# Kernel tuning notes

Measured on AMD Instinct MI355X. Metric: run time of the kernel, lower is better.

## Reference

```python
import jax, jax.numpy as jnp
import numpy as np

B, S, HID = 4, 1024, 4096
NH, NKV, HD = 32, 8, 128
FF = 11008
EPS = 1e-6
THETA = 10000.0


def rms_norm(x, w, eps=EPS):
    v = jnp.mean(jnp.square(x), axis=-1, keepdims=True)
    return x * jax.lax.rsqrt(v + eps) * w


def rotate_half(x):
    x1, x2 = jnp.split(x, 2, axis=-1)
    return jnp.concatenate([-x2, x1], axis=-1)


def rope_cos_sin(position_ids, head_dim=HD, theta=THETA):
    inv_freq = 1.0 / (theta ** (jnp.arange(0, head_dim, 2, dtype=jnp.float32) / head_dim))
    freqs = position_ids.astype(jnp.float32)[..., None] * inv_freq  # [B,S,HD/2]
    emb = jnp.concatenate([freqs, freqs], axis=-1)  # [B,S,HD]
    return jnp.cos(emb)[:, None, :, :], jnp.sin(emb)[:, None, :, :]  # [B,1,S,HD]


def setup_inputs() -> dict:
    key = jax.random.key(0)
    ks = jax.random.split(key, 9)
    sc = 0.02
    pos = jnp.tile(jnp.arange(S, dtype=jnp.int64 if jax.config.jax_enable_x64 else jnp.int32)[None, :], (B, 1))
    causal = jnp.tril(jnp.ones((S, S), dtype=bool))
    mask = jnp.where(causal, 0.0, -1e9).astype(jnp.float32)[None, None]  # [1,1,S,S]
    return {
        "hidden_states": jax.random.normal(ks[0], (B * S, HID), jnp.float32),
        "position_ids": pos,
        "attn_mask": mask,
        "Wq": jax.random.normal(ks[1], (HID, NH * HD), jnp.float32) * sc,
        "Wk": jax.random.normal(ks[2], (HID, NKV * HD), jnp.float32) * sc,
        "Wv": jax.random.normal(ks[3], (HID, NKV * HD), jnp.float32) * sc,
        "Wo": jax.random.normal(ks[4], (NH * HD, HID), jnp.float32) * sc,
        "ln1_w": jnp.ones((HID,), jnp.float32),
        "ln2_w": jnp.ones((HID,), jnp.float32),
        "w_gate": jax.random.normal(ks[5], (HID, FF), jnp.float32) * sc,
        "w_up": jax.random.normal(ks[6], (HID, FF), jnp.float32) * sc,
        "w_down": jax.random.normal(ks[7], (FF, HID), jnp.float32) * sc,
    }


def reference(hidden_states, position_ids, attn_mask, Wq, Wk, Wv, Wo, ln1_w, ln2_w, w_gate, w_up, w_down):
    residual = hidden_states
    h = rms_norm(hidden_states, ln1_w)

    # QKV projections on flat tokens, then reshape per train partition
    q = (h @ Wq).reshape(B, S, NH, HD).transpose(0, 2, 1, 3)     # [B,NH,S,HD]
    k = (h @ Wk).reshape(B, S, NKV, HD).transpose(0, 2, 1, 3)    # [B,NKV,S,HD]
    v = (h @ Wv).reshape(B, S, NKV, HD).transpose(0, 2, 1, 3)

    cos, sin = rope_cos_sin(position_ids)
    q = q * cos + rotate_half(q) * sin
    k = k * cos + rotate_half(k) * sin

    n_rep = NH // NKV
    k = jnp.repeat(k, n_rep, axis=1)  # [B,NH,S,HD]
    v = jnp.repeat(v, n_rep, axis=1)

    scores = jnp.einsum('bhqd,bhkd->bhqk', q, k) / np.sqrt(HD)
    scores = scores + attn_mask
    # softmax in fp32 as in the source
    probs = jax.nn.softmax(scores.astype(jnp.float32), axis=-1).astype(q.dtype)
    attn = jnp.einsum('bhqk,bhkd->bhqd', probs, v)               # [B,NH,S,HD]
    attn = attn.transpose(0, 2, 1, 3).reshape(B * S, NH * HD)
    h = attn @ Wo

    h = residual + h
    residual = h
    h2 = rms_norm(h, ln2_w)
    mlp = (jax.nn.silu(h2 @ w_gate) * (h2 @ w_up)) @ w_down
    return residual + mlp
```

## Files before the change

kernel.cpp:

```cpp
#include <hip/hip_runtime.h>

#define DEVINL __device__ __forceinline__

typedef unsigned short u16;
typedef __attribute__((ext_vector_type(8))) short bf16x8;
typedef __attribute__((ext_vector_type(4))) float f32x4;
typedef __attribute__((ext_vector_type(4))) unsigned short u16x4;


DEVINL float bf2f(u16 u) { union { unsigned i; float f; } x; x.i = ((unsigned)u) << 16; return x.f; }
DEVINL u16 f2bf(float f) {
  union { float f; unsigned i; } x; x.f = f;
  unsigned r = x.i + 0x7fffu + ((x.i >> 16) & 1u);
  return (u16)(r >> 16);
}

DEVINL void async16(u16* lds, const u16* g) {
  __builtin_amdgcn_global_load_lds((const __attribute__((address_space(1))) unsigned*)g,
                                   (__attribute__((address_space(3))) unsigned*)lds, 16, 0, 0);
}

struct CJob { const float* in; u16* out; int K, N, ntiles; };

DEVINL void conv_one(const float* __restrict__ in, u16* __restrict__ out,
                     int K, int N, int tile, int t, float (*tl)[65]) {
  int tn = N >> 6;
  int kt = tile / tn;
  int k0 = kt << 6, n0 = (tile - kt*tn) << 6;
  int r = t >> 4, c4 = (t & 15) << 2;
  #pragma unroll
  for (int it = 0; it < 4; it++) {
    int row = r + it*16;
    f32x4 v = *(const f32x4*)(in + (size_t)(k0 + row)*N + n0 + c4);
    tl[row][c4+0] = v[0]; tl[row][c4+1] = v[1];
    tl[row][c4+2] = v[2]; tl[row][c4+3] = v[3];
  }
  __syncthreads();
  #pragma unroll
  for (int it = 0; it < 4; it++) {
    int nrow = r + it*16;
    u16x4 ov;
    #pragma unroll
    for (int e = 0; e < 4; e++) ov[e] = f2bf(tl[c4+e][nrow]);
    *(u16x4*)(out + (size_t)(n0 + nrow)*K + k0 + c4) = ov;
  }
  __syncthreads();
}

__global__ __launch_bounds__(256) void conv3(CJob j0, CJob j1, CJob j2) {
  __shared__ float tl[64][65];
  int ntot = j0.ntiles + j1.ntiles + j2.ntiles;
  for (int g = blockIdx.x; g < ntot; g += gridDim.x) {
    const float* in; u16* out; int K, N, tile;
    if (g < j0.ntiles)                 { in = j0.in; out = j0.out; K = j0.K; N = j0.N; tile = g; }
    else if (g < j0.ntiles + j1.ntiles){ in = j1.in; out = j1.out; K = j1.K; N = j1.N; tile = g - j0.ntiles; }
    else                               { in = j2.in; out = j2.out; K = j2.K; N = j2.N; tile = g - j0.ntiles - j1.ntiles; }
    conv_one(in, out, K, N, tile, threadIdx.x, tl);
  }
}

__global__ __launch_bounds__(256) void conv_t(const float* __restrict__ in,
                                              u16* __restrict__ out, int K, int N) {
  __shared__ float tl[64][65];
  int tile = blockIdx.y * gridDim.x + blockIdx.x;
  conv_one(in, out, K, N, tile, threadIdx.x, tl);
}

__global__ __launch_bounds__(256) void rmsnorm_kernel(const float* __restrict__ x,
                                                      const float* __restrict__ w,
                                                      u16* __restrict__ out) {
  int row = blockIdx.x, t = threadIdx.x;
  const float* xr = x + (size_t)row * 4096;
  f32x4 v[4];
  float ss = 0.f;
  #pragma unroll
  for (int i = 0; i < 4; i++) {
    v[i] = *(const f32x4*)(xr + (t + 256*i)*4);
    ss += v[i][0]*v[i][0] + v[i][1]*v[i][1] + v[i][2]*v[i][2] + v[i][3]*v[i][3];
  }
  #pragma unroll
  for (int d = 1; d < 64; d <<= 1) ss += __shfl_xor(ss, d, 64);
  __shared__ float ps[4];
  if ((t & 63) == 0) ps[t >> 6] = ss;
  __syncthreads();
  float scale = rsqrtf((ps[0]+ps[1]+ps[2]+ps[3]) * (1.f/4096.f) + 1e-6f);
  #pragma unroll
  for (int i = 0; i < 4; i++) {
    f32x4 wv = *(const f32x4*)(w + (t + 256*i)*4);
    u16x4 o;
    #pragma unroll
    for (int e = 0; e < 4; e++) o[e] = f2bf(v[i][e] * scale * wv[e]);
    *(u16x4*)(out + (size_t)row*4096 + (t + 256*i)*4) = o;
  }
}

__global__ __launch_bounds__(256) void rope_kernel(u16* __restrict__ q, u16* __restrict__ k, int kstr) {
  int tok = blockIdx.x;
  int s = tok & 1023;
  __shared__ float cs[64], sn[64];
  int t = threadIdx.x;
  if (t < 64) {
    float inv = __expf(-(float)t * 0.14391156934f);
    float ang = (float)s * inv;
    cs[t] = cosf(ang); sn[t] = sinf(ang);
  }
  __syncthreads();
  const float qscale = 0.08838834764831845f;
  size_t qbase = (size_t)tok * 4096;
  #pragma unroll
  for (int it = 0; it < 8; it++) {
    int item = t + it*256; int h = item >> 6, j = item & 63;
    size_t i0 = qbase + h*128 + j;
    float x1 = bf2f(q[i0]), x2 = bf2f(q[i0+64]);
    float c = cs[j], si = sn[j];
    q[i0]    = f2bf((x1*c - x2*si) * qscale);
    q[i0+64] = f2bf((x2*c + x1*si) * qscale);
  }
  size_t kbase = (size_t)tok * kstr;
  #pragma unroll
  for (int it = 0; it < 2; it++) {
    int item = t + it*256; int h = item >> 6, j = item & 63;
    size_t i0 = kbase + h*128 + j;
    float x1 = bf2f(k[i0]), x2 = bf2f(k[i0+64]);
    float c = cs[j], si = sn[j];
    k[i0]    = f2bf(x1*c - x2*si);
    k[i0+64] = f2bf(x2*c + x1*si);
  }
}

__global__ __launch_bounds__(256) void vtrans(const u16* __restrict__ v, u16* __restrict__ vt, int vstr) {
  __shared__ u16 tile[32][33];
  int bh = blockIdx.z; int b = bh >> 3, kvh = bh & 7;
  int d0 = blockIdx.x << 5, s0 = blockIdx.y << 5;
  int tx = threadIdx.x, ty = threadIdx.y;
  for (int r = ty; r < 32; r += 8)
    tile[r][tx] = v[(size_t)(b*1024 + s0 + r)*vstr + kvh*128 + d0 + tx];
  __syncthreads();
  for (int r = ty; r < 32; r += 8)
    vt[(size_t)((b*8 + kvh)*128 + d0 + r)*1024 + s0 + tx] = tile[tx][r];
}

template<int EPI>
__global__ __launch_bounds__(256, 2) void gemm_bt(
    const u16* __restrict__ A, const u16* __restrict__ Bt,
    void* __restrict__ Cv, const float* __restrict__ resid,
    const u16* __restrict__ gate, int M, int N, int K) {
  __shared__ u16 As[128*64];
  __shared__ u16 Bs[128*64];
  int nwg = gridDim.x;
  int bid = (int)blockIdx.x;
  int cpx = nwg >> 3;
  int swz = (bid & 7) * cpx + (bid >> 3);
  int mt = M >> 7;
  int m0 = (swz % mt) << 7;
  int n0 = (swz / mt) << 7;
  int tid = threadIdx.x;
  int lane = tid & 63, wave = tid >> 6;
  int wm = wave >> 1, wn = wave & 1;

  f32x4 acc[4][4];
  f32x4 zero = {0.f, 0.f, 0.f, 0.f};
  #pragma unroll
  for (int i = 0; i < 4; i++)
    #pragma unroll
    for (int j = 0; j < 4; j++) acc[i][j] = zero;

  int arow[4], acolb[4];
  #pragma unroll
  for (int i = 0; i < 4; i++) {
    int c = i*256 + tid;
    arow[i]  = c >> 3;
    acolb[i] = ((c & 7) * 16) ^ ((arow[i] & 7) << 4);
  }

  int nsteps = K >> 6;
  for (int t = 0; t < nsteps; t++) {
    int k0 = t << 6;
    #pragma unroll
    for (int i = 0; i < 4; i++) {
      async16(As + i*2048 + wave*512, A  + (size_t)(m0 + arow[i])*K + k0 + (acolb[i] >> 1));
      async16(Bs + i*2048 + wave*512, Bt + (size_t)(n0 + arow[i])*K + k0 + (acolb[i] >> 1));
    }
    __syncthreads();
    #pragma unroll
    for (int ks = 0; ks < 2; ks++) {
      bf16x8 af[4], bfr[4];
      int c2 = (ks*32 + (lane >> 4)*8) * 2;
      #pragma unroll
      for (int mf = 0; mf < 4; mf++) {
        int r = wm*64 + mf*16 + (lane & 15);
        af[mf] = *(const bf16x8*)(As + r*64 + ((c2 ^ ((r & 7) << 4)) >> 1));
      }
      #pragma unroll
      for (int nf = 0; nf < 4; nf++) {
        int r = wn*64 + nf*16 + (lane & 15);
        bfr[nf] = *(const bf16x8*)(Bs + r*64 + ((c2 ^ ((r & 7) << 4)) >> 1));
      }
      #pragma unroll
      for (int mf = 0; mf < 4; mf++)
        #pragma unroll
        for (int nf = 0; nf < 4; nf++)
          acc[mf][nf] = __builtin_amdgcn_mfma_f32_16x16x32_bf16(af[mf], bfr[nf], acc[mf][nf], 0, 0, 0);
    }
    __syncthreads();
  }

  #pragma unroll
  for (int mf = 0; mf < 4; mf++)
    #pragma unroll
    for (int nf = 0; nf < 4; nf++)
      #pragma unroll
      for (int j = 0; j < 4; j++) {
        int rr = m0 + wm*64 + mf*16 + (lane >> 4)*4 + j;
        int cc = n0 + wn*64 + nf*16 + (lane & 15);
        size_t idx = (size_t)rr * N + cc;
        float v = acc[mf][nf][j];
        if constexpr (EPI == 0) {
          ((u16*)Cv)[idx] = f2bf(v);
        } else if constexpr (EPI == 1) {
          ((float*)Cv)[idx] = v + resid[idx];
        } else {
          float g = bf2f(gate[idx]);
          float sg = g / (1.f + __expf(-g));
          ((u16*)Cv)[idx] = f2bf(sg * v);
        }
      }
}

#define SB0() __builtin_amdgcn_sched_barrier(0)
#define BAR() __builtin_amdgcn_s_barrier()
#define LGKM(n) do { SB0(); asm volatile("s_waitcnt lgkmcnt(" #n ")" ::: "memory"); SB0(); } while (0)
#define VMC(n)  do { SB0(); asm volatile("s_waitcnt vmcnt(" #n ")"  ::: "memory"); SB0(); } while (0)
#define MFMAQ(qm, qn, AF, BQ) do { \
  __builtin_amdgcn_s_setprio(1); \
  _Pragma("unroll") for (int mf_ = 0; mf_ < 4; mf_++) \
  _Pragma("unroll") for (int nf_ = 0; nf_ < 2; nf_++) \
  _Pragma("unroll") for (int ks_ = 0; ks_ < 2; ks_++) \
    acc[(qm)*4+mf_][(qn)*2+nf_] = __builtin_amdgcn_mfma_f32_16x16x32_bf16( \
        AF[mf_][ks_], BQ[nf_][ks_], acc[(qm)*4+mf_][(qn)*2+nf_], 0, 0, 0); \
  __builtin_amdgcn_s_setprio(0); } while (0)

template<int KC, int EPI>
__global__ __launch_bounds__(512, 2) void gemm256(
    const u16* __restrict__ A, const u16* __restrict__ Bt,
    void* __restrict__ Cv, const float* __restrict__ resid,
    const u16* __restrict__ gate, int M, int N, int G,
    const float* __restrict__ cvin, u16* __restrict__ cvout, int cvK, int cvN, int cvTiles) {
  extern __shared__ u16 lds[];
  int bid = (int)blockIdx.x;
  int tid = threadIdx.x;

  if (bid >= G) {
    int cb = bid - G, CB = (int)gridDim.x - G;
    int h = tid >> 8, t = tid & 255;
    float (*tl)[65] = (float(*)[65])((char*)lds + h*16896);
    int pairs = cvTiles >> 1;
    for (int p = cb; p < pairs; p += CB)
      conv_one(cvin, cvout, cvK, cvN, 2*p + h, t, tl);
    return;
  }

  int cpx = G >> 3;
  int swz = (bid & 7) * cpx + (bid >> 3);
  int mt = M >> 8;
  int m0 = (swz % mt) << 8;
  int n0 = (swz / mt) << 8;
  int lane = tid & 63, wave = tid >> 6;
  int wm = wave >> 2, wn = wave & 3;

  f32x4 acc[8][4];
  f32x4 zero = {0.f, 0.f, 0.f, 0.f};
  #pragma unroll
  for (int i = 0; i < 8; i++)
    #pragma unroll
    for (int j = 0; j < 4; j++) acc[i][j] = zero;

  int sCol = ((lane & 7) ^ (lane >> 3)) << 3;
  int aRow = (wave >> 2)*128 + (wave & 3)*16 + (lane >> 3);
  int bRow = (wave >> 1)*64  + (wave & 1)*16 + (lane >> 3);
  const u16* gA = A  + (size_t)(m0 + aRow) * KC + sCol;
  const u16* gB = Bt + (size_t)(n0 + bRow) * KC + sCol;
  constexpr size_t K8 = (size_t)8 * KC, K32 = (size_t)32 * KC, K64 = (size_t)64 * KC;

  int rA = lane & 15;
  int acol0 = (((lane >> 4)    ) ^ (rA & 7)) << 3;
  int acol1 = (((lane >> 4) + 4) ^ (rA & 7)) << 3;

  bf16x8 afA[4][2], afB[4][2], b0[2][2], b1[2][2];

  auto stageAq = [&](int buf, int qm, int k0) {
    u16* d = lds + buf*32768 + qm*8192 + wave*1024;
    const u16* s = gA + (size_t)qm*K64 + k0;
    async16(d, s); async16(d + 512, s + K8);
  };
  auto stageBq = [&](int buf, int qn, int k0) {
    u16* d = lds + buf*32768 + 16384 + qn*8192 + wave*1024;
    const u16* s = gB + (size_t)qn*K32 + k0;
    async16(d, s); async16(d + 512, s + K8);
  };
  auto loadAq = [&](int buf, int qm, bf16x8 (&af)[4][2]) {
    const u16* base = lds + buf*32768 + qm*8192 + wm*4096 + rA*64;
    #pragma unroll
    for (int mf = 0; mf < 4; mf++) {
      af[mf][0] = *(const bf16x8*)(base + mf*1024 + acol0);
      af[mf][1] = *(const bf16x8*)(base + mf*1024 + acol1);
    }
  };
  auto loadBq = [&](int buf, int qn, bf16x8 (&bq)[2][2]) {
    const u16* base = lds + buf*32768 + 16384 + qn*8192 + wn*2048 + rA*64;
    #pragma unroll
    for (int nf = 0; nf < 2; nf++) {
      bq[nf][0] = *(const bf16x8*)(base + nf*1024 + acol0);
      bq[nf][1] = *(const bf16x8*)(base + nf*1024 + acol1);
    }
  };

  constexpr int nt = KC >> 6;
  constexpr int IT = nt/2 - 1;

  stageAq(0, 0, 0); stageBq(0, 0, 0); stageBq(0, 1, 0); stageAq(0, 1, 0);
  VMC(4);
  stageAq(1, 0, 64); stageBq(1, 0, 64); stageBq(1, 1, 64);
  VMC(6);
  BAR();

  #pragma unroll 1
  for (int it = 0; it < IT; it++) {
    int kc = it*128;
    loadAq(0, 0, afA); loadBq(0, 0, b0); stageAq(1, 1, kc + 64);
    LGKM(8); BAR(); LGKM(0);
    MFMAQ(0, 0, afA, b0);
    SB0(); BAR();
    loadBq(0, 1, b1); stageAq(0, 0, kc + 128);
    BAR(); LGKM(0);
    MFMAQ(0, 1, afA, b1);
    SB0(); BAR();
    loadAq(0, 1, afB); stageBq(0, 0, kc + 128);
    BAR(); LGKM(0);
    MFMAQ(1, 0, afB, b0);
    SB0(); BAR();
    stageBq(0, 1, kc + 128);
    BAR();
    MFMAQ(1, 1, afB, b1);
    VMC(6); BAR();
    loadAq(1, 0, afA); loadBq(1, 0, b0); stageAq(0, 1, kc + 128);
    LGKM(8); BAR(); LGKM(0);
    MFMAQ(0, 0, afA, b0);
    SB0(); BAR();
    loadBq(1, 1, b1); stageAq(1, 0, kc + 192);
    BAR(); LGKM(0);
    MFMAQ(0, 1, afA, b1);
    SB0(); BAR();
    loadAq(1, 1, afB); stageBq(1, 0, kc + 192);
    BAR(); LGKM(0);
    MFMAQ(1, 0, afB, b0);
    SB0(); BAR();
    stageBq(1, 1, kc + 192);
    BAR();
    MFMAQ(1, 1, afB, b1);
    VMC(6); BAR();
  }

  {
    int kc = IT*128;
    loadAq(0, 0, afA); loadBq(0, 0, b0); stageAq(1, 1, kc + 64);
    LGKM(8); BAR(); LGKM(0);
    MFMAQ(0, 0, afA, b0);
    SB0(); BAR();
    loadBq(0, 1, b1);
    BAR(); LGKM(0);
    MFMAQ(0, 1, afA, b1);
    SB0(); BAR();
    loadAq(0, 1, afB);
    BAR(); LGKM(0);
    MFMAQ(1, 0, afB, b0);
    SB0(); BAR();
    MFMAQ(1, 1, afB, b1);
    VMC(0); BAR();
    loadAq(1, 0, afA); loadBq(1, 0, b0); SB0();
    loadBq(1, 1, b1); SB0();
    loadAq(1, 1, afB); SB0();
    LGKM(12); MFMAQ(0, 0, afA, b0);
    LGKM(8);  MFMAQ(0, 1, afA, b1);
    LGKM(0);  MFMAQ(1, 0, afB, b0);
    MFMAQ(1, 1, afB, b1);
  }

  #pragma unroll
  for (int mf = 0; mf < 8; mf++)
    #pragma unroll
    for (int nf = 0; nf < 4; nf++)
      #pragma unroll
      for (int j = 0; j < 4; j++) {
        int rr = m0 + wm*128 + mf*16 + (lane >> 4)*4 + j;
        int cc = n0 + wn*64 + nf*16 + (lane & 15);
        size_t idx = (size_t)rr * N + cc;
        float v = acc[mf][nf][j];
        if constexpr (EPI == 0) {
          ((u16*)Cv)[idx] = f2bf(v);
        } else if constexpr (EPI == 1) {
          ((float*)Cv)[idx] = v + resid[idx];
        } else {
          float g = bf2f(gate[idx]);
          float sg = g / (1.f + __expf(-g));
          ((u16*)Cv)[idx] = f2bf(sg * v);
        }
      }
}

__global__ __launch_bounds__(256, 4) void attn_kernel(
    const u16* __restrict__ q, const u16* __restrict__ k,
    const u16* __restrict__ vt, u16* __restrict__ out,
    CJob j0, CJob j1, CJob j2, int kstr) {
  __shared__ __align__(16) u16 shm[20480];
  u16* Ks = shm;
  u16* Vs = shm + 8192;
  u16* Ps = shm + 16384;
  int bid = blockIdx.x;

  if (bid >= 2048) {
    int cb = bid - 2048, CB = (int)gridDim.x - 2048;
    float (*tl)[65] = (float(*)[65])shm;
    int ntot = j0.ntiles + j1.ntiles + j2.ntiles;
    for (int g = cb; g < ntot; g += CB) {
      const float* in; u16* outp; int K, N, tile;
      if (g < j0.ntiles)                  { in = j0.in; outp = j0.out; K = j0.K; N = j0.N; tile = g; }
      else if (g < j0.ntiles + j1.ntiles) { in = j1.in; outp = j1.out; K = j1.K; N = j1.N; tile = g - j0.ntiles; }
      else                                { in = j2.in; outp = j2.out; K = j2.K; N = j2.N; tile = g - j0.ntiles - j1.ntiles; }
      conv_one(in, outp, K, N, tile, threadIdx.x, tl);
    }
    return;
  }

  int qt = bid & 15;
  int h  = (bid >> 4) & 31;
  int b  = bid >> 9;
  int kvh = h >> 2;
  int tid = threadIdx.x, lane = tid & 63, wave = tid >> 6;
  int q0 = qt << 6;

  bf16x8 qf[4];
  {
    const u16* qb_ = q + (size_t)(b*1024 + q0 + wave*16 + (lane & 15))*4096 + h*128 + (lane >> 4)*8;
    #pragma unroll
    for (int ks = 0; ks < 4; ks++) qf[ks] = *(const bf16x8*)(qb_ + ks*32);
  }
  f32x4 o[8];
  f32x4 zero = {0.f,0.f,0.f,0.f};
  #pragma unroll
  for (int i = 0; i < 8; i++) o[i] = zero;
  float m[4] = {-1e30f,-1e30f,-1e30f,-1e30f};
  float l[4] = {0.f,0.f,0.f,0.f};

  int kr[4], kc[4], vr[4], vc[4];
  #pragma unroll
  for (int i = 0; i < 4; i++) {
    int c = i*256 + tid;
    kr[i] = c >> 4; kc[i] = ((c & 15)*16) ^ ((kr[i] & 7) << 4);
    vr[i] = c >> 3; vc[i] = ((c & 7)*16)  ^ ((vr[i] & 7) << 4);
  }

  for (int t = 0; t <= qt; t++) {
    int kv0 = t << 6;
    #pragma unroll
    for (int i = 0; i < 4; i++) {
      async16(Ks + i*2048 + wave*512, k  + (size_t)(b*1024 + kv0 + kr[i])*kstr + kvh*128 + (kc[i] >> 1));
      async16(Vs + i*2048 + wave*512, vt + (size_t)((b*8 + kvh)*128 + vr[i])*1024 + kv0 + (vc[i] >> 1));
    }
    __syncthreads();

    f32x4 s[4];
    #pragma unroll
    for (int nf = 0; nf < 4; nf++) {
      s[nf] = zero;
      #pragma unroll
      for (int ks = 0; ks < 4; ks++) {
        int r = nf*16 + (lane & 15);
        int c2 = (ks*32 + (lane >> 4)*8)*2;
        bf16x8 kf = *(const bf16x8*)(Ks + r*128 + ((c2 ^ ((r & 7) << 4)) >> 1));
        s[nf] = __builtin_amdgcn_mfma_f32_16x16x32_bf16(qf[ks], kf, s[nf], 0, 0, 0);
      }
    }
    if (t == qt) {
      #pragma unroll
      for (int nf = 0; nf < 4; nf++)
        #pragma unroll
        for (int j = 0; j < 4; j++) {
          int cc = nf*16 + (lane & 15);
          int rr = wave*16 + (lane >> 4)*4 + j;
          if (cc > rr) s[nf][j] = -1e30f;
        }
    }
    #pragma unroll
    for (int j = 0; j < 4; j++) {
      float mx = fmaxf(fmaxf(s[0][j], s[1][j]), fmaxf(s[2][j], s[3][j]));
      #pragma unroll
      for (int d = 1; d < 16; d <<= 1) mx = fmaxf(mx, __shfl_xor(mx, d, 64));
      float mn = fmaxf(m[j], mx);
      float f = __expf(m[j] - mn);
      m[j] = mn;
      float ssum = 0.f;
      #pragma unroll
      for (int nf = 0; nf < 4; nf++) {
        float p = __expf(s[nf][j] - mn);
        s[nf][j] = p; ssum += p;
      }
      #pragma unroll
      for (int d = 1; d < 16; d <<= 1) ssum += __shfl_xor(ssum, d, 64);
      l[j] = l[j]*f + ssum;
      #pragma unroll
      for (int nf = 0; nf < 8; nf++) o[nf][j] *= f;
    }
    #pragma unroll
    for (int nf = 0; nf < 4; nf++)
      #pragma unroll
      for (int j = 0; j < 4; j++) {
        int rr = (lane >> 4)*4 + j;
        int cb2 = ((nf*16 + (lane & 15))*2) ^ ((rr & 7) << 4);
        Ps[wave*1024 + rr*64 + (cb2 >> 1)] = f2bf(s[nf][j]);
      }
    #pragma unroll
    for (int ks2 = 0; ks2 < 2; ks2++) {
      int mr = lane & 15;
      int c2 = (ks2*32 + (lane >> 4)*8)*2;
      bf16x8 pa = *(const bf16x8*)(Ps + wave*1024 + mr*64 + ((c2 ^ ((mr & 7) << 4)) >> 1));
      #pragma unroll
      for (int nf = 0; nf < 8; nf++) {
        int d = nf*16 + (lane & 15);
        bf16x8 vf = *(const bf16x8*)(Vs + d*64 + ((c2 ^ ((d & 7) << 4)) >> 1));
        o[nf] = __builtin_amdgcn_mfma_f32_16x16x32_bf16(pa, vf, o[nf], 0, 0, 0);
      }
    }
    __syncthreads();
  }

  float inv[4];
  #pragma unroll
  for (int j = 0; j < 4; j++) inv[j] = 1.f / l[j];
  u16* ob = out + (size_t)(b*1024 + q0 + wave*16)*4096 + h*128;
  #pragma unroll
  for (int nf = 0; nf < 8; nf++)
    #pragma unroll
    for (int j = 0; j < 4; j++) {
      int rr = (lane >> 4)*4 + j;
      int cc = nf*16 + (lane & 15);
      ob[(size_t)rr*4096 + cc] = f2bf(o[nf][j] * inv[j]);
    }
}

extern "C" void kernel_launch(void* const* d_in, const int* in_sizes, int n_in,
                              void* d_out, int out_size, void* d_ws, size_t ws_size,
                              hipStream_t stream) {
  (void)in_sizes; (void)n_in; (void)out_size;
  const float* hidden = (const float*)d_in[0];
  const float* Wq  = (const float*)d_in[3];
  const float* Wk  = (const float*)d_in[4];
  const float* Wv  = (const float*)d_in[5];
  const float* Wo  = (const float*)d_in[6];
  const float* ln1 = (const float*)d_in[7];
  const float* ln2 = (const float*)d_in[8];
  const float* Wg  = (const float*)d_in[9];
  const float* Wu  = (const float*)d_in[10];
  const float* Wd  = (const float*)d_in[11];
  float* out = (float*)d_out;

  hipFuncSetAttribute((const void*)gemm256<4096,0>,  hipFuncAttributeMaxDynamicSharedMemorySize, 131072);
  hipFuncSetAttribute((const void*)gemm256<4096,1>,  hipFuncAttributeMaxDynamicSharedMemorySize, 131072);
  hipFuncSetAttribute((const void*)gemm256<4096,2>,  hipFuncAttributeMaxDynamicSharedMemorySize, 131072);
  hipFuncSetAttribute((const void*)gemm256<11008,1>, hipFuncAttributeMaxDynamicSharedMemorySize, 131072);

  char* ws = (char*)d_ws;
  size_t off = 0;
  auto alloc = [&](size_t b) { char* p = ws + off; off += (b + 4095) & ~(size_t)4095; return p; };

  u16*  wqkvT = (u16*)alloc(50331648);
  u16*  woT   = (u16*)alloc(33554432);
  u16*  wgT   = (u16*)alloc(90177536);
  u16*  wuT   = (u16*)alloc(90177536);
  u16*  h1    = (u16*)alloc(33554432);
  u16*  qb    = (u16*)alloc(33554432);
  u16*  kvb   = (u16*)alloc(16777216);
  u16*  vtb   = (u16*)alloc(8388608);
  float* hmid = (float*)alloc(67108864);
  u16*  gb    = (u16*)alloc(90177536);
  bool fused = off <= ws_size;

  dim3 blk(256);
  if (fused) {
    u16* wqT  = wqkvT;
    u16* wkvT = wqkvT + 16777216;
    u16* wkT  = wkvT;
    u16* wvT  = wkvT + 4194304;
    u16* wdT  = wgT;
    CJob Jq{Wq, wqT, 4096, 4096, 4096}, Jk{Wk, wkT, 4096, 1024, 1024}, Jv{Wv, wvT, 4096, 1024, 1024};
    CJob Jo{Wo, woT, 4096, 4096, 4096}, Jg{Wg, wgT, 4096, 11008, 11008}, Ju{Wu, wuT, 4096, 11008, 11008};

    conv3<<<2048, blk, 0, stream>>>(Jq, Jk, Jv);
    rmsnorm_kernel<<<4096, blk, 0, stream>>>(hidden, ln1, h1);
    gemm256<4096,0><<<256, 512, 131072, stream>>>(h1, wqT, qb, nullptr, nullptr, 4096, 4096, 256,
                                                  nullptr, nullptr, 0, 0, 0);
    gemm_bt<0><<<512, blk, 0, stream>>>(h1, wkvT, kvb, nullptr, nullptr, 4096, 2048, 4096);
    rope_kernel<<<4096, blk, 0, stream>>>(qb, kvb, 2048);
    vtrans<<<dim3(4, 32, 32), dim3(32, 8), 0, stream>>>(kvb + 1024, vtb, 2048);
    attn_kernel<<<2048 + 1024, blk, 0, stream>>>(qb, kvb, vtb, h1, Jo, Jg, Ju, 2048);
    gemm256<4096,1><<<256, 512, 131072, stream>>>(h1, woT, hmid, hidden, nullptr, 4096, 4096, 256,
                                                  nullptr, nullptr, 0, 0, 0);
    rmsnorm_kernel<<<4096, blk, 0, stream>>>(hmid, ln2, qb);
    gemm256<4096,0><<<688, 512, 131072, stream>>>(qb, wgT, gb, nullptr, nullptr, 4096, 11008, 688,
                                                  nullptr, nullptr, 0, 0, 0);
    gemm256<4096,2><<<688 + 344, 512, 131072, stream>>>(qb, wuT, gb, nullptr, gb, 4096, 11008, 688,
                                                        Wd, wdT, 11008, 4096, 11008);
    gemm256<11008,1><<<256, 512, 131072, stream>>>(gb, wdT, out, hmid, nullptr, 4096, 4096, 256,
                                                   nullptr, nullptr, 0, 0, 0);
  } else {
    off = 0;
    u16*  W1   = (u16*)alloc(90177536);
    u16*  h1s  = (u16*)alloc(33554432);
    u16*  qbs  = (u16*)alloc(33554432);
    u16*  kvbs = (u16*)alloc(16777216);
    u16*  vtbs = (u16*)alloc(8388608);
    float* hmids = (float*)alloc(67108864);
    u16*  gbs  = (u16*)alloc(90177536);
    if (off > ws_size) return;
    u16* wqT  = W1;
    u16* wkvT = W1 + 16777216;
    conv_t<<<dim3(64, 64),  blk, 0, stream>>>(Wq, wqT, 4096, 4096);
    conv_t<<<dim3(16, 64),  blk, 0, stream>>>(Wk, wkvT, 4096, 1024);
    conv_t<<<dim3(16, 64),  blk, 0, stream>>>(Wv, wkvT + 4194304, 4096, 1024);
    rmsnorm_kernel<<<4096, blk, 0, stream>>>(hidden, ln1, h1s);
    gemm256<4096,0><<<256, 512, 131072, stream>>>(h1s, wqT, qbs, nullptr, nullptr, 4096, 4096, 256,
                                                  nullptr, nullptr, 0, 0, 0);
    gemm_bt<0><<<512, blk, 0, stream>>>(h1s, wkvT, kvbs, nullptr, nullptr, 4096, 2048, 4096);
    rope_kernel<<<4096, blk, 0, stream>>>(qbs, kvbs, 2048);
    vtrans<<<dim3(4, 32, 32), dim3(32, 8), 0, stream>>>(kvbs + 1024, vtbs, 2048);
    CJob J0{nullptr, nullptr, 0, 64, 0};
    attn_kernel<<<2048, blk, 0, stream>>>(qbs, kvbs, vtbs, h1s, J0, J0, J0, 2048);
    conv_t<<<dim3(64, 64), blk, 0, stream>>>(Wo, W1, 4096, 4096);
    gemm256<4096,1><<<256, 512, 131072, stream>>>(h1s, W1, hmids, hidden, nullptr, 4096, 4096, 256,
                                                  nullptr, nullptr, 0, 0, 0);
    rmsnorm_kernel<<<4096, blk, 0, stream>>>(hmids, ln2, qbs);
    conv_t<<<dim3(172, 64), blk, 0, stream>>>(Wg, W1, 4096, 11008);
    gemm256<4096,0><<<688, 512, 131072, stream>>>(qbs, W1, gbs, nullptr, nullptr, 4096, 11008, 688,
                                                  nullptr, nullptr, 0, 0, 0);
    conv_t<<<dim3(172, 64), blk, 0, stream>>>(Wu, W1, 4096, 11008);
    gemm256<4096,2><<<688, 512, 131072, stream>>>(qbs, W1, gbs, nullptr, gbs, 4096, 11008, 688,
                                                  nullptr, nullptr, 0, 0, 0);
    conv_t<<<dim3(64, 172), blk, 0, stream>>>(Wd, W1, 11008, 4096);
    gemm256<11008,1><<<256, 512, 131072, stream>>>(gbs, W1, out, hmids, nullptr, 4096, 4096, 256,
                                                   nullptr, nullptr, 0, 0, 0);
  }
}
```

Before: 1.665 ms.

## Fuse gate and up projections into one GEMM with interleaved weights

Gate and up weights are converted into a single interleaved buffer, alternating 32-row blocks, so that one GEMM of width 22016 produces both projections in the same tile. A new epilogue applies SiLU(gate)*up directly from registers. This removes the separate gate GEMM, its bf16 write of the gate result and the later read-back. The cost is a larger combined weight buffer and a reshuffled workspace layout, with the down-weight conversion now placed in the QKV buffer region.

```diff
diff --git a/kernel.cpp b/kernel.cpp
--- a/kernel.cpp
+++ b/kernel.cpp
@@ -20,10 +20,10 @@
                                    (__attribute__((address_space(3))) unsigned*)lds, 16, 0, 0);
 }
 
-struct CJob { const float* in; u16* out; int K, N, ntiles; };
+struct CJob { const float* in; u16* out; int K, N, ntiles; int mode; };
 
 DEVINL void conv_one(const float* __restrict__ in, u16* __restrict__ out,
-                     int K, int N, int tile, int t, float (*tl)[65]) {
+                     int K, int N, int tile, int t, float (*tl)[65], int mode) {
   int tn = N >> 6;
   int kt = tile / tn;
   int k0 = kt << 6, n0 = (tile - kt*tn) << 6;
@@ -42,7 +42,10 @@
     u16x4 ov;
     #pragma unroll
     for (int e = 0; e < 4; e++) ov[e] = f2bf(tl[c4+e][nrow]);
-    *(u16x4*)(out + (size_t)(n0 + nrow)*K + k0 + c4) = ov;
+    int orow = n0 + nrow;
+    if (mode == 1)      orow = ((orow >> 5) << 6) + (orow & 31);
+    else if (mode == 2) orow = ((orow >> 5) << 6) + 32 + (orow & 31);
+    *(u16x4*)(out + (size_t)orow*K + k0 + c4) = ov;
   }
   __syncthreads();
 }
@@ -51,11 +54,12 @@
   __shared__ float tl[64][65];
   int ntot = j0.ntiles + j1.ntiles + j2.ntiles;
   for (int g = blockIdx.x; g < ntot; g += gridDim.x) {
-    const float* in; u16* out; int K, N, tile;
-    if (g < j0.ntiles)                 { in = j0.in; out = j0.out; K = j0.K; N = j0.N; tile = g; }
-    else if (g < j0.ntiles + j1.ntiles){ in = j1.in; out = j1.out; K = j1.K; N = j1.N; tile = g - j0.ntiles; }
-    else                               { in = j2.in; out = j2.out; K = j2.K; N = j2.N; tile = g - j0.ntiles - j1.ntiles; }
-    conv_one(in, out, K, N, tile, threadIdx.x, tl);
+    CJob* jp;
+    int tile;
+    if (g < j0.ntiles)                 { jp = &j0; tile = g; }
+    else if (g < j0.ntiles + j1.ntiles){ jp = &j1; tile = g - j0.ntiles; }
+    else                               { jp = &j2; tile = g - j0.ntiles - j1.ntiles; }
+    conv_one(jp->in, jp->out, jp->K, jp->N, tile, threadIdx.x, tl, jp->mode);
   }
 }
 
@@ -63,7 +67,7 @@
                                               u16* __restrict__ out, int K, int N) {
   __shared__ float tl[64][65];
   int tile = blockIdx.y * gridDim.x + blockIdx.x;
-  conv_one(in, out, K, N, tile, threadIdx.x, tl);
+  conv_one(in, out, K, N, tile, threadIdx.x, tl, 0);
 }
 
 __global__ __launch_bounds__(256) void rmsnorm_kernel(const float* __restrict__ x,
@@ -245,7 +249,7 @@
     const u16* __restrict__ A, const u16* __restrict__ Bt,
     void* __restrict__ Cv, const float* __restrict__ resid,
     const u16* __restrict__ gate, int M, int N, int G,
-    const float* __restrict__ cvin, u16* __restrict__ cvout, int cvK, int cvN, int cvTiles) {
+    const float* __restrict__ cvin, u16* __restrict__ cvout, int cvK, int cvN, int cvTiles, int cvMode) {
   extern __shared__ u16 lds[];
   int bid = (int)blockIdx.x;
   int tid = threadIdx.x;
@@ -256,7 +260,7 @@
     float (*tl)[65] = (float(*)[65])((char*)lds + h*16896);
     int pairs = cvTiles >> 1;
     for (int p = cb; p < pairs; p += CB)
-      conv_one(cvin, cvout, cvK, cvN, 2*p + h, t, tl);
+      conv_one(cvin, cvout, cvK, cvN, 2*p + h, t, tl, cvMode);
     return;
   }
 
@@ -386,26 +390,42 @@
     MFMAQ(1, 1, afB, b1);
   }
 
-  #pragma unroll
-  for (int mf = 0; mf < 8; mf++)
-    #pragma unroll
-    for (int nf = 0; nf < 4; nf++)
-      #pragma unroll
-      for (int j = 0; j < 4; j++) {
-        int rr = m0 + wm*128 + mf*16 + (lane >> 4)*4 + j;
-        int cc = n0 + wn*64 + nf*16 + (lane & 15);
-        size_t idx = (size_t)rr * N + cc;
-        float v = acc[mf][nf][j];
-        if constexpr (EPI == 0) {
-          ((u16*)Cv)[idx] = f2bf(v);
-        } else if constexpr (EPI == 1) {
-          ((float*)Cv)[idx] = v + resid[idx];
-        } else {
-          float g = bf2f(gate[idx]);
+  if constexpr (EPI == 3) {
+    int colb = (n0 >> 1) + wn*32 + (lane & 15);
+    #pragma unroll
+    for (int mf = 0; mf < 8; mf++)
+      #pragma unroll
+      for (int nf = 0; nf < 2; nf++)
+        #pragma unroll
+        for (int j = 0; j < 4; j++) {
+          int rr = m0 + wm*128 + mf*16 + (lane >> 4)*4 + j;
+          float g = acc[mf][nf][j];
+          float u = acc[mf][nf+2][j];
           float sg = g / (1.f + __expf(-g));
-          ((u16*)Cv)[idx] = f2bf(sg * v);
+          ((u16*)Cv)[(size_t)rr * 11008 + colb + nf*16] = f2bf(sg * u);
         }
-      }
+  } else {
+    #pragma unroll
+    for (int mf = 0; mf < 8; mf++)
+      #pragma unroll
+      for (int nf = 0; nf < 4; nf++)
+        #pragma unroll
+        for (int j = 0; j < 4; j++) {
+          int rr = m0 + wm*128 + mf*16 + (lane >> 4)*4 + j;
+          int cc = n0 + wn*64 + nf*16 + (lane & 15);
+          size_t idx = (size_t)rr * N + cc;
+          float v = acc[mf][nf][j];
+          if constexpr (EPI == 0) {
+            ((u16*)Cv)[idx] = f2bf(v);
+          } else if constexpr (EPI == 1) {
+            ((float*)Cv)[idx] = v + resid[idx];
+          } else if constexpr (EPI == 2) {
+            float g = bf2f(gate[idx]);
+            float sg = g / (1.f + __expf(-g));
+            ((u16*)Cv)[idx] = f2bf(sg * v);
+          }
+        }
+  }
 }
 
 __global__ __launch_bounds__(256, 4) void attn_kernel(
@@ -423,11 +443,11 @@
     float (*tl)[65] = (float(*)[65])shm;
     int ntot = j0.ntiles + j1.ntiles + j2.ntiles;
     for (int g = cb; g < ntot; g += CB) {
-      const float* in; u16* outp; int K, N, tile;
-      if (g < j0.ntiles)                  { in = j0.in; outp = j0.out; K = j0.K; N = j0.N; tile = g; }
-      else if (g < j0.ntiles + j1.ntiles) { in = j1.in; outp = j1.out; K = j1.K; N = j1.N; tile = g - j0.ntiles; }
-      else                                { in = j2.in; outp = j2.out; K = j2.K; N = j2.N; tile = g - j0.ntiles - j1.ntiles; }
-      conv_one(in, outp, K, N, tile, threadIdx.x, tl);
+      CJob* jp; int tile;
+      if (g < j0.ntiles)                  { jp = &j0; tile = g; }
+      else if (g < j0.ntiles + j1.ntiles) { jp = &j1; tile = g - j0.ntiles; }
+      else                                { jp = &j2; tile = g - j0.ntiles - j1.ntiles; }
+      conv_one(jp->in, jp->out, jp->K, jp->N, tile, threadIdx.x, tl, jp->mode);
     }
     return;
   }
@@ -567,6 +587,7 @@
   hipFuncSetAttribute((const void*)gemm256<4096,0>,  hipFuncAttributeMaxDynamicSharedMemorySize, 131072);
   hipFuncSetAttribute((const void*)gemm256<4096,1>,  hipFuncAttributeMaxDynamicSharedMemorySize, 131072);
   hipFuncSetAttribute((const void*)gemm256<4096,2>,  hipFuncAttributeMaxDynamicSharedMemorySize, 131072);
+  hipFuncSetAttribute((const void*)gemm256<4096,3>,  hipFuncAttributeMaxDynamicSharedMemorySize, 131072);
   hipFuncSetAttribute((const void*)gemm256<11008,1>, hipFuncAttributeMaxDynamicSharedMemorySize, 131072);
 
   char* ws = (char*)d_ws;
@@ -575,8 +596,8 @@
 
   u16*  wqkvT = (u16*)alloc(50331648);
   u16*  woT   = (u16*)alloc(33554432);
-  u16*  wgT   = (u16*)alloc(90177536);
-  u16*  wuT   = (u16*)alloc(90177536);
+  (void)alloc(8388608);
+  u16*  wguT  = (u16*)alloc(180355072);
   u16*  h1    = (u16*)alloc(33554432);
   u16*  qb    = (u16*)alloc(33554432);
   u16*  kvb   = (u16*)alloc(16777216);
@@ -591,27 +612,26 @@
     u16* wkvT = wqkvT + 16777216;
     u16* wkT  = wkvT;
     u16* wvT  = wkvT + 4194304;
-    u16* wdT  = wgT;
-    CJob Jq{Wq, wqT, 4096, 4096, 4096}, Jk{Wk, wkT, 4096, 1024, 1024}, Jv{Wv, wvT, 4096, 1024, 1024};
-    CJob Jo{Wo, woT, 4096, 4096, 4096}, Jg{Wg, wgT, 4096, 11008, 11008}, Ju{Wu, wuT, 4096, 11008, 11008};
+    u16* wdT  = wqkvT;
+    CJob Jq{Wq, wqT, 4096, 4096, 4096, 0}, Jk{Wk, wkT, 4096, 1024, 1024, 0}, Jv{Wv, wvT, 4096, 1024, 1024, 0};
+    CJob Jo{Wo, woT, 4096, 4096, 4096, 0};
+    CJob Jg{Wg, wguT, 4096, 11008, 11008, 1}, Ju{Wu, wguT, 4096, 11008, 11008, 2};
 
     conv3<<<2048, blk, 0, stream>>>(Jq, Jk, Jv);
     rmsnorm_kernel<<<4096, blk, 0, stream>>>(hidden, ln1, h1);
     gemm256<4096,0><<<256, 512, 131072, stream>>>(h1, wqT, qb, nullptr, nullptr, 4096, 4096, 256,
-                                                  nullptr, nullptr, 0, 0, 0);
+                                                  nullptr, nullptr, 0, 0, 0, 0);
     gemm_bt<0><<<512, blk, 0, stream>>>(h1, wkvT, kvb, nullptr, nullptr, 4096, 2048, 4096);
     rope_kernel<<<4096, blk, 0, stream>>>(qb, kvb, 2048);
     vtrans<<<dim3(4, 32, 32), dim3(32, 8), 0, stream>>>(kvb + 1024, vtb, 2048);
     attn_kernel<<<2048 + 1024, blk, 0, stream>>>(qb, kvb, vtb, h1, Jo, Jg, Ju, 2048);
     gemm256<4096,1><<<256, 512, 131072, stream>>>(h1, woT, hmid, hidden, nullptr, 4096, 4096, 256,
-                                                  nullptr, nullptr, 0, 0, 0);
+                                                  nullptr, nullptr, 0, 0, 0, 0);
     rmsnorm_kernel<<<4096, blk, 0, stream>>>(hmid, ln2, qb);
-    gemm256<4096,0><<<688, 512, 131072, stream>>>(qb, wgT, gb, nullptr, nullptr, 4096, 11008, 688,
-                                                  nullptr, nullptr, 0, 0, 0);
-    gemm256<4096,2><<<688 + 344, 512, 131072, stream>>>(qb, wuT, gb, nullptr, gb, 4096, 11008, 688,
-                                                        Wd, wdT, 11008, 4096, 11008);
+    gemm256<4096,3><<<1376 + 344, 512, 131072, stream>>>(qb, wguT, gb, nullptr, nullptr, 4096, 11008, 1376,
+                                                         Wd, wdT, 11008, 4096, 11008, 0);
     gemm256<11008,1><<<256, 512, 131072, stream>>>(gb, wdT, out, hmid, nullptr, 4096, 4096, 256,
-                                                   nullptr, nullptr, 0, 0, 0);
+                                                   nullptr, nullptr, 0, 0, 0, 0);
   } else {
     off = 0;
     u16*  W1   = (u16*)alloc(90177536);
@@ -629,24 +649,24 @@
     conv_t<<<dim3(16, 64),  blk, 0, stream>>>(Wv, wkvT + 4194304, 4096, 1024);
     rmsnorm_kernel<<<4096, blk, 0, stream>>>(hidden, ln1, h1s);
     gemm256<4096,0><<<256, 512, 131072, stream>>>(h1s, wqT, qbs, nullptr, nullptr, 4096, 4096, 256,
-                                                  nullptr, nullptr, 0, 0, 0);
+                                                  nullptr, nullptr, 0, 0, 0, 0);
     gemm_bt<0><<<512, blk, 0, stream>>>(h1s, wkvT, kvbs, nullptr, nullptr, 4096, 2048, 4096);
     rope_kernel<<<4096, blk, 0, stream>>>(qbs, kvbs, 2048);
     vtrans<<<dim3(4, 32, 32), dim3(32, 8), 0, stream>>>(kvbs + 1024, vtbs, 2048);
-    CJob J0{nullptr, nullptr, 0, 64, 0};
+    CJob J0{nullptr, nullptr, 0, 64, 0, 0};
     attn_kernel<<<2048, blk, 0, stream>>>(qbs, kvbs, vtbs, h1s, J0, J0, J0, 2048);
     conv_t<<<dim3(64, 64), blk, 0, stream>>>(Wo, W1, 4096, 4096);
     gemm256<4096,1><<<256, 512, 131072, stream>>>(h1s, W1, hmids, hidden, nullptr, 4096, 4096, 256,
-                                                  nullptr, nullptr, 0, 0, 0);
+                                                  nullptr, nullptr, 0, 0, 0, 0);
     rmsnorm_kernel<<<4096, blk, 0, stream>>>(hmids, ln2, qbs);
     conv_t<<<dim3(172, 64), blk, 0, stream>>>(Wg, W1, 4096, 11008);
     gemm256<4096,0><<<688, 512, 131072, stream>>>(qbs, W1, gbs, nullptr, nullptr, 4096, 11008, 688,
-                                                  nullptr, nullptr, 0, 0, 0);
+                                                  nullptr, nullptr, 0, 0, 0, 0);
     conv_t<<<dim3(172, 64), blk, 0, stream>>>(Wu, W1, 4096, 11008);
     gemm256<4096,2><<<688, 512, 131072, stream>>>(qbs, W1, gbs, nullptr, gbs, 4096, 11008, 688,
-                                                  nullptr, nullptr, 0, 0, 0);
+                                                  nullptr, nullptr, 0, 0, 0, 0);
     conv_t<<<dim3(64, 172), blk, 0, stream>>>(Wd, W1, 11008, 4096);
     gemm256<11008,1><<<256, 512, 131072, stream>>>(gbs, W1, out, hmids, nullptr, 4096, 4096, 256,
-                                                   nullptr, nullptr, 0, 0, 0);
-  }
-}
+                                                   nullptr, nullptr, 0, 0, 0, 0);
+  }
+}
```

After: 1.625 ms. 2.4% less time.
